# Kernel tuning notes

Measured on AMD Instinct MI355X. Metric: run time of the kernel, lower is better.

The kernel has to match this reference:

```python
import jax, jax.numpy as jnp
import numpy as np

N, D = 8192, 1024


def setup_inputs() -> dict:
    key = jax.random.key(0)
    k1, k2 = jax.random.split(key)
    source = jax.random.normal(k1, (N, D), dtype=jnp.float32)
    target = jax.random.normal(k2, (N, D), dtype=jnp.float32)
    return {"source": source, "target": target}


def reference(source, target):
    # delta: [N, D]; loss = mean over all N*N entries of delta @ delta.T
    delta = source - target
    gram = jnp.matmul(delta, delta.T)  # [N, N]
    return jnp.mean(gram)
```

## Files before the change

### kernel.cpp

```cpp
#include <hip/hip_runtime.h>


#define MMD_N 8192
#define MMD_D 1024
#define CS_BLOCKS 256
#define CS_THREADS 1024
#define TEAMS 4
#define ROWS_PER_TEAM 8
#define INV_N2 1.4901161193847656e-8f

__global__ __launch_bounds__(CS_THREADS) void mmd_colsum(
    const float* __restrict__ src, const float* __restrict__ tgt,
    float* __restrict__ ws) {
    const int tid  = threadIdx.x;
    const int team = tid >> 8;
    const int col4 = tid & 255;
    const int row0 = blockIdx.x * (TEAMS * ROWS_PER_TEAM) + team * ROWS_PER_TEAM;
    const float4* s4 = reinterpret_cast<const float4*>(src);
    const float4* t4 = reinterpret_cast<const float4*>(tgt);

    float4 acc = make_float4(0.f, 0.f, 0.f, 0.f);
#pragma unroll
    for (int r = 0; r < ROWS_PER_TEAM; ++r) {
        const int idx = (row0 + r) * (MMD_D / 4) + col4;
        float4 s = s4[idx];
        float4 t = t4[idx];
        acc.x += s.x - t.x;
        acc.y += s.y - t.y;
        acc.z += s.z - t.z;
        acc.w += s.w - t.w;
    }

    __shared__ float4 red[TEAMS][256];
    red[team][col4] = acc;
    __syncthreads();
    if (tid < 256) {
        float4 a = red[0][tid];
        float4 b = red[1][tid];
        float4 c = red[2][tid];
        float4 d = red[3][tid];
        float4 tot;
        tot.x = (a.x + b.x) + (c.x + d.x);
        tot.y = (a.y + b.y) + (c.y + d.y);
        tot.z = (a.z + b.z) + (c.z + d.z);
        tot.w = (a.w + b.w) + (c.w + d.w);
        reinterpret_cast<float4*>(ws)[blockIdx.x * 256 + tid] = tot;
    }
}

__global__ __launch_bounds__(256) void mmd_finale(
    const float* __restrict__ ws, float* __restrict__ out) {
    const int tid  = threadIdx.x;
    const int j    = tid >> 6;
    const int lane = tid & 63;
    const int c    = blockIdx.x * 4 + j;
    const float4* w4 = reinterpret_cast<const float4*>(ws);

    float4 acc = make_float4(0.f, 0.f, 0.f, 0.f);
#pragma unroll
    for (int k = 0; k < CS_BLOCKS / 64; ++k) {
        float4 v = w4[(lane + 64 * k) * 256 + c];
        acc.x += v.x; acc.y += v.y; acc.z += v.z; acc.w += v.w;
    }
    for (int off = 32; off > 0; off >>= 1) {
        acc.x += __shfl_down(acc.x, off, 64);
        acc.y += __shfl_down(acc.y, off, 64);
        acc.z += __shfl_down(acc.z, off, 64);
        acc.w += __shfl_down(acc.w, off, 64);
    }
    if (lane == 0) {
        float sq = acc.x * acc.x + acc.y * acc.y + acc.z * acc.z + acc.w * acc.w;
        atomicAdd(out, sq * INV_N2);
    }
}

extern "C" void kernel_launch(void* const* d_in, const int* in_sizes, int n_in,
                              void* d_out, int out_size, void* d_ws, size_t ws_size,
                              hipStream_t stream) {
    const float* src = (const float*)d_in[0];
    const float* tgt = (const float*)d_in[1];
    float* out = (float*)d_out;
    float* ws = (float*)d_ws;

    hipMemsetAsync(out, 0, sizeof(float), stream);
    mmd_colsum<<<CS_BLOCKS, CS_THREADS, 0, stream>>>(src, tgt, ws);
    mmd_finale<<<64, 256, 0, stream>>>(ws, out);
}
```

Measured before the change: 25.55 us.

## Fuse column-sum and finale into one cooperative kernel with grid sync

Replaces the memset plus two-kernel sequence with a single cooperative launch. The kernel zeroes the output itself, computes per-block column partial sums, waits at a grid-wide barrier, then each of the 256 blocks reduces one float4 column group across all blocks and atomically adds its squared sum. The aim is to remove the launch and memset overhead. In exchange it takes on the cost of a grid barrier and depends on all 256×1024-thread blocks being co-resident. A restructured two-kernel path with 512-thread blocks and loads batched before the arithmetic is kept as a fallback in case the cooperative launch fails.

```diff
diff --git a/kernel.cpp b/kernel.cpp
--- a/kernel.cpp
+++ b/kernel.cpp
@@ -1,4 +1,7 @@
 #include <hip/hip_runtime.h>
+#include <hip/hip_cooperative_groups.h>
+
+namespace cg = cooperative_groups;
 
 
 #define MMD_N 8192
@@ -9,15 +12,17 @@
 #define ROWS_PER_TEAM 8
 #define INV_N2 1.4901161193847656e-8f
 
-__global__ __launch_bounds__(CS_THREADS) void mmd_colsum(
+__global__ __launch_bounds__(CS_THREADS) void mmd_fused(
     const float* __restrict__ src, const float* __restrict__ tgt,
-    float* __restrict__ ws) {
+    float* __restrict__ ws, float* __restrict__ out) {
     const int tid  = threadIdx.x;
     const int team = tid >> 8;
     const int col4 = tid & 255;
     const int row0 = blockIdx.x * (TEAMS * ROWS_PER_TEAM) + team * ROWS_PER_TEAM;
     const float4* s4 = reinterpret_cast<const float4*>(src);
     const float4* t4 = reinterpret_cast<const float4*>(tgt);
+
+    if (blockIdx.x == 0 && tid == 0) out[0] = 0.f;
 
     float4 acc = make_float4(0.f, 0.f, 0.f, 0.f);
 #pragma unroll
@@ -46,9 +51,84 @@
         tot.w = (a.w + b.w) + (c.w + d.w);
         reinterpret_cast<float4*>(ws)[blockIdx.x * 256 + tid] = tot;
     }
+
+    cg::this_grid().sync();
+
+    const float4* w4 = reinterpret_cast<const float4*>(ws);
+    float4 colacc = make_float4(0.f, 0.f, 0.f, 0.f);
+    if (tid < 256) {
+        colacc = w4[tid * 256 + blockIdx.x];
+    }
+    const int lane = tid & 63;
+    for (int off = 32; off > 0; off >>= 1) {
+        colacc.x += __shfl_down(colacc.x, off, 64);
+        colacc.y += __shfl_down(colacc.y, off, 64);
+        colacc.z += __shfl_down(colacc.z, off, 64);
+        colacc.w += __shfl_down(colacc.w, off, 64);
+    }
+    __shared__ float4 part[4];
+    if (tid < 256 && lane == 0) part[tid >> 6] = colacc;
+    __syncthreads();
+    if (tid == 0) {
+        float4 a = part[0], b = part[1], c = part[2], d = part[3];
+        float4 tot;
+        tot.x = (a.x + b.x) + (c.x + d.x);
+        tot.y = (a.y + b.y) + (c.y + d.y);
+        tot.z = (a.z + b.z) + (c.z + d.z);
+        tot.w = (a.w + b.w) + (c.w + d.w);
+        float sq = tot.x * tot.x + tot.y * tot.y + tot.z * tot.z + tot.w * tot.w;
+        atomicAdd(out, sq * INV_N2);
+    }
 }
 
-__global__ __launch_bounds__(256) void mmd_finale(
+#define FB_BLOCKS 512
+#define FB_THREADS 512
+#define FB_TEAMS 2
+#define FB_ROWS_PER_TEAM 8
+
+__global__ __launch_bounds__(FB_THREADS) void mmd_colsum_fb(
+    const float* __restrict__ src, const float* __restrict__ tgt,
+    float* __restrict__ ws, float* __restrict__ out) {
+    const int tid  = threadIdx.x;
+    const int team = tid >> 8;
+    const int col4 = tid & 255;
+    const int row0 = blockIdx.x * (FB_TEAMS * FB_ROWS_PER_TEAM) + team * FB_ROWS_PER_TEAM;
+    const float4* s4 = reinterpret_cast<const float4*>(src);
+    const float4* t4 = reinterpret_cast<const float4*>(tgt);
+
+    if (blockIdx.x == 0 && tid == 0) out[0] = 0.f;
+
+    float4 s[FB_ROWS_PER_TEAM], t[FB_ROWS_PER_TEAM];
+#pragma unroll
+    for (int r = 0; r < FB_ROWS_PER_TEAM; ++r)
+        s[r] = s4[(row0 + r) * (MMD_D / 4) + col4];
+#pragma unroll
+    for (int r = 0; r < FB_ROWS_PER_TEAM; ++r)
+        t[r] = t4[(row0 + r) * (MMD_D / 4) + col4];
+
+    float4 acc = make_float4(0.f, 0.f, 0.f, 0.f);
+#pragma unroll
+    for (int r = 0; r < FB_ROWS_PER_TEAM; ++r) {
+        acc.x += s[r].x - t[r].x;
+        acc.y += s[r].y - t[r].y;
+        acc.z += s[r].z - t[r].z;
+        acc.w += s[r].w - t[r].w;
+    }
+
+    __shared__ float4 red[FB_TEAMS][256];
+    red[team][col4] = acc;
+    __syncthreads();
+    if (tid < 256) {
+        float4 a = red[0][tid];
+        float4 b = red[1][tid];
+        float4 tot;
+        tot.x = a.x + b.x; tot.y = a.y + b.y;
+        tot.z = a.z + b.z; tot.w = a.w + b.w;
+        reinterpret_cast<float4*>(ws)[blockIdx.x * 256 + tid] = tot;
+    }
+}
+
+__global__ __launch_bounds__(256) void mmd_finale_fb(
     const float* __restrict__ ws, float* __restrict__ out) {
     const int tid  = threadIdx.x;
     const int j    = tid >> 6;
@@ -58,7 +138,7 @@
 
     float4 acc = make_float4(0.f, 0.f, 0.f, 0.f);
 #pragma unroll
-    for (int k = 0; k < CS_BLOCKS / 64; ++k) {
+    for (int k = 0; k < FB_BLOCKS / 64; ++k) {
         float4 v = w4[(lane + 64 * k) * 256 + c];
         acc.x += v.x; acc.y += v.y; acc.z += v.z; acc.w += v.w;
     }
@@ -82,7 +162,11 @@
     float* out = (float*)d_out;
     float* ws = (float*)d_ws;
 
-    hipMemsetAsync(out, 0, sizeof(float), stream);
-    mmd_colsum<<<CS_BLOCKS, CS_THREADS, 0, stream>>>(src, tgt, ws);
-    mmd_finale<<<64, 256, 0, stream>>>(ws, out);
+    void* args[] = {(void*)&src, (void*)&tgt, (void*)&ws, (void*)&out};
+    hipError_t err = hipLaunchCooperativeKernel(
+        (const void*)mmd_fused, dim3(CS_BLOCKS), dim3(CS_THREADS), args, 0, stream);
+    if (err != hipSuccess) {
+        mmd_colsum_fb<<<FB_BLOCKS, FB_THREADS, 0, stream>>>(src, tgt, ws, out);
+        mmd_finale_fb<<<64, 256, 0, stream>>>(ws, out);
+    }
 }
```

Result: slower. 59.72 us (+133.8%).
